# Kernel tuning notes

Hardware: AMD Instinct MI355X
Metric: run time of the kernel (lower is better)

Reference implementation:

```python
import jax, jax.numpy as jnp
import numpy as np

N_NODES = 100000
N_EDGES = 3200000
N_GRAPHS = 1000


def transformer_conv(x, src, dst, Wq, bq, Wk, bk, Wv, bv, Ws, bs, num_nodes):
    """PyG TransformerConv, heads=1, concat=True, root_weight=True, beta=False.
    Message flows src -> dst; softmax over incoming edges of each dst node."""
    d = Wq.shape[1]
    q = x @ Wq + bq                                   # [N, d]
    k = x @ Wk + bk                                   # [N, d]
    v = x @ Wv + bv                                   # [N, d]
    s = (q[dst] * k[src]).sum(-1) / jnp.sqrt(jnp.asarray(d, x.dtype))  # [E]
    smax = jax.ops.segment_max(s, dst, num_segments=num_nodes)         # [N]
    smax = jnp.where(jnp.isfinite(smax), smax, 0.0)   # nodes with no in-edges
    e = jnp.exp(s - smax[dst])                        # [E]
    denom = jax.ops.segment_sum(e, dst, num_segments=num_nodes)        # [N]
    alpha = e / jnp.maximum(denom[dst], 1e-16)        # [E]
    agg = jax.ops.segment_sum(alpha[:, None] * v[src], dst, num_segments=num_nodes)
    return agg + x @ Ws + bs                          # skip connection (lin_skip)


def setup_inputs() -> dict:
    key = jax.random.key(0)
    ks = jax.random.split(key, 20)
    x = jax.random.normal(ks[0], (N_NODES, 11), dtype=jnp.float32)
    edge_index = jax.random.randint(ks[1], (2, N_EDGES), 0, N_NODES, dtype=jnp.int64)
    batch = jnp.sort(jax.random.randint(ks[2], (N_NODES,), 0, N_GRAPHS, dtype=jnp.int64))

    def lin(k, fan_in, fan_out):
        kw, kb = jax.random.split(k)
        s = 1.0 / np.sqrt(fan_in)
        W = jax.random.uniform(kw, (fan_in, fan_out), jnp.float32, -s, s)
        b = jax.random.uniform(kb, (fan_out,), jnp.float32, -s, s)
        return W, b

    Wq1, bq1 = lin(ks[3], 11, 16); Wk1, bk1 = lin(ks[4], 11, 16)
    Wv1, bv1 = lin(ks[5], 11, 16); Ws1, bs1 = lin(ks[6], 11, 16)
    Wq2, bq2 = lin(ks[7], 16, 32); Wk2, bk2 = lin(ks[8], 16, 32)
    Wv2, bv2 = lin(ks[9], 16, 32); Ws2, bs2 = lin(ks[10], 16, 32)
    Wf1, bf1 = lin(ks[11], 32, 64)
    Wf2, bf2 = lin(ks[12], 64, 1)
    return dict(x=x, edge_index=edge_index, batch=batch,
                Wq1=Wq1, bq1=bq1, Wk1=Wk1, bk1=bk1, Wv1=Wv1, bv1=bv1, Ws1=Ws1, bs1=bs1,
                Wq2=Wq2, bq2=bq2, Wk2=Wk2, bk2=bk2, Wv2=Wv2, bv2=bv2, Ws2=Ws2, bs2=bs2,
                Wf1=Wf1, bf1=bf1, Wf2=Wf2, bf2=bf2)


def reference(x, edge_index, batch,
              Wq1, bq1, Wk1, bk1, Wv1, bv1, Ws1, bs1,
              Wq2, bq2, Wk2, bk2, Wv2, bv2, Ws2, bs2,
              Wf1, bf1, Wf2, bf2):
    src, dst = edge_index[0], edge_index[1]
    h = jax.nn.relu(transformer_conv(x, src, dst, Wq1, bq1, Wk1, bk1, Wv1, bv1, Ws1, bs1, N_NODES))
    h = jax.nn.relu(transformer_conv(h, src, dst, Wq2, bq2, Wk2, bk2, Wv2, bv2, Ws2, bs2, N_NODES))
    # global_mean_pool over graphs
    sums = jax.ops.segment_sum(h, batch, num_segments=N_GRAPHS)            # [G, 32]
    counts = jax.ops.segment_sum(jnp.ones((h.shape[0],), h.dtype), batch, num_segments=N_GRAPHS)
    g = sums / jnp.maximum(counts, 1.0)[:, None]
    g = jax.nn.relu(g @ Wf1 + bf1)
    return g @ Wf2 + bf2                                                   # [G, 1]
```

## Files before the change

kernel.cpp:

```cpp
#include <hip/hip_runtime.h>
#include <hip/hip_bf16.h>
#include <math.h>

#define N_NODES  100000
#define N_EDGES  3200000
#define N_GRAPHS 1000
#define NBKT ((N_NODES + 255) >> 8)
#define BCAP 9216
#define PCHUNK 4096
#define EPT (PCHUNK / 256)

__device__ __forceinline__ unsigned short f2bf(float f) {
    unsigned u = __float_as_uint(f);
    return (unsigned short)((u + 0x7FFFu + ((u >> 16) & 1u)) >> 16);
}
__device__ __forceinline__ void unpack2(unsigned u, float& a, float& b) {
    a = __uint_as_float(u << 16);
    b = __uint_as_float(u & 0xFFFF0000u);
}

__global__ void detect_kernel(const long long* __restrict__ idx, int* __restrict__ flag) {
    int t = threadIdx.x;
    unsigned long long hi = ((unsigned long long)idx[t]) >> 32;
    unsigned long long any = __ballot(hi != 0ull);
    if (t == 0) *flag = (any == 0ull) ? 1 : 0;
}

__global__ __launch_bounds__(256)
void init_kernel(unsigned* __restrict__ bcur, float* __restrict__ pool,
                 float* __restrict__ cnt) {
    int t = blockIdx.x * blockDim.x + threadIdx.x;
    if (t < NBKT)         bcur[t] = (unsigned)t * BCAP;
    if (t < N_GRAPHS*32)  pool[t] = 0.f;
    if (t < N_GRAPHS)     cnt[t]  = 0.f;
}

__global__ __launch_bounds__(256)
void partition_kernel(const int* __restrict__ idx32, const long long* __restrict__ idx64,
                      const int* __restrict__ flag,
                      unsigned* __restrict__ bcur, unsigned* __restrict__ srtp) {
    __shared__ unsigned       sbuf[PCHUNK];
    __shared__ unsigned short sbkt[PCHUNK];
    __shared__ unsigned lhist[NBKT];
    __shared__ unsigned lscan[512];
    __shared__ unsigned gbase[NBKT];
    const int is64 = *flag;
    const int t = threadIdx.x;
    const int base = blockIdx.x * PCHUNK;
    const int nval = min(PCHUNK, N_EDGES - base);

    for (int b = t; b < NBKT; b += 256) lhist[b] = 0u;
    __syncthreads();

    unsigned pr[EPT]; unsigned short br[EPT]; unsigned short rr[EPT];
    #pragma unroll
    for (int r = 0; r < EPT; ++r) {
        int e = base + r * 256 + t;
        br[r] = 0xFFFF;
        if (e < N_EDGES) {
            int s = is64 ? (int)idx64[e]           : idx32[e];
            int d = is64 ? (int)idx64[N_EDGES + e] : idx32[N_EDGES + e];
            unsigned bk = ((unsigned)d) >> 8;
            pr[r] = (((unsigned)d & 255u) << 17) | (unsigned)s;
            br[r] = (unsigned short)bk;
            rr[r] = (unsigned short)atomicAdd(&lhist[bk], 1u);
        }
    }
    __syncthreads();

    lscan[t]       = (t < NBKT)       ? lhist[t]       : 0u;
    lscan[t + 256] = (t + 256 < NBKT) ? lhist[t + 256] : 0u;
    __syncthreads();
    for (int off = 1; off < 512; off <<= 1) {
        unsigned v0 = (t >= off)       ? lscan[t - off]       : 0u;
        unsigned v1 = (t + 256 >= off) ? lscan[t + 256 - off] : 0u;
        __syncthreads();
        lscan[t] += v0; lscan[t + 256] += v1;
        __syncthreads();
    }

    for (int b = t; b < NBKT; b += 256) {
        unsigned c = lhist[b];
        if (c) gbase[b] = atomicAdd(&bcur[b], c);
    }

    #pragma unroll
    for (int r = 0; r < EPT; ++r) {
        if (br[r] != 0xFFFF) {
            unsigned b = br[r];
            unsigned slot = lscan[b] - lhist[b] + rr[r];
            sbuf[slot] = pr[r];
            sbkt[slot] = (unsigned short)b;
        }
    }
    __syncthreads();

    for (int slot = t; slot < nval; slot += 256) {
        unsigned p = sbuf[slot];
        unsigned b = sbkt[slot];
        unsigned lst = lscan[b] - lhist[b];
        srtp[gbase[b] + ((unsigned)slot - lst)] = p;
    }
}

__global__ __launch_bounds__(256)
void build_kernel(unsigned* __restrict__ srtp, const unsigned* __restrict__ bcur,
                  int* __restrict__ row_start, int* __restrict__ row_end) {
    __shared__ unsigned sbuf[BCAP];
    __shared__ int      sdst[BCAP];
    __shared__ unsigned ldeg[256];
    __shared__ unsigned lsc[256];
    __shared__ int      lcur[256];
    const int b = blockIdx.x;
    const int t = threadIdx.x;
    const int segbase = b * BCAP;
    const int cntb = min((int)bcur[b] - segbase, BCAP);

    ldeg[t] = 0u;
    __syncthreads();
    for (int e = t; e < cntb; e += 256) {
        unsigned p = srtp[segbase + e];
        sbuf[e] = p;
        atomicAdd(&ldeg[p >> 17], 1u);
    }
    __syncthreads();
    lsc[t] = ldeg[t];
    __syncthreads();
    for (int off = 1; off < 256; off <<= 1) {
        unsigned v = (t >= off) ? lsc[t - off] : 0u;
        __syncthreads();
        lsc[t] += v;
        __syncthreads();
    }
    int excl = (int)(lsc[t] - ldeg[t]);
    int node = (b << 8) + t;
    if (node < N_NODES) {
        row_start[node] = segbase + excl;
        row_end[node]   = segbase + excl + (int)ldeg[t];
    }
    lcur[t] = excl;
    __syncthreads();
    for (int e = t; e < cntb; e += 256) {
        unsigned p = sbuf[e];
        int pos = atomicAdd(&lcur[p >> 17], 1);
        sdst[pos] = (int)(p & 0x1FFFFu);
    }
    __syncthreads();

    const int wave = t >> 6, lane = t & 63;
    for (int n = wave; n < 256; n += 4) {
        int len = (int)ldeg[n];
        if (len < 2 || len > 64) continue;
        int lofs = (int)(lsc[n] - ldeg[n]);
        int v = (lane < len) ? sdst[lofs + lane] : 0x7FFFFFFF;
        #pragma unroll
        for (int k = 2; k <= 64; k <<= 1) {
            #pragma unroll
            for (int j = k >> 1; j > 0; j >>= 1) {
                int pv = __shfl_xor(v, j, 64);
                bool up    = (lane & k) == 0;
                bool lower = (lane & j) == 0;
                int mn = min(v, pv), mx = max(v, pv);
                v = (up == lower) ? mn : mx;
            }
        }
        if (lane < len) sdst[lofs + lane] = v;
    }
    __syncthreads();
    for (int e = t; e < cntb; e += 256)
        srtp[segbase + e] = (unsigned)sdst[e];
}

template <int IN, int OUT>
__global__ __launch_bounds__(256)
void lin_kernel(const float* __restrict__ x,
                const float* __restrict__ Wq, const float* __restrict__ bq,
                const float* __restrict__ Wk, const float* __restrict__ bk,
                const float* __restrict__ Wv, const float* __restrict__ bv,
                const float* __restrict__ Ws, const float* __restrict__ bs,
                float scale,
                float* __restrict__ q, unsigned short* __restrict__ kv,
                float* __restrict__ sk, int n)
{
    __shared__ float w[4 * IN * OUT];
    __shared__ float b[4 * OUT];
    for (int t = threadIdx.x; t < IN * OUT; t += blockDim.x) {
        w[t]            = Wq[t];
        w[IN*OUT + t]   = Wk[t];
        w[2*IN*OUT + t] = Wv[t];
        w[3*IN*OUT + t] = Ws[t];
    }
    for (int t = threadIdx.x; t < OUT; t += blockDim.x) {
        b[t]         = bq[t];
        b[OUT + t]   = bk[t];
        b[2*OUT + t] = bv[t];
        b[3*OUT + t] = bs[t];
    }
    __syncthreads();

    for (int i = blockIdx.x * blockDim.x + threadIdx.x; i < n;
         i += gridDim.x * blockDim.x) {
        float xi[IN];
        #pragma unroll
        for (int r = 0; r < IN; ++r) xi[r] = x[(size_t)i * IN + r];

        #pragma unroll
        for (int j = 0; j < OUT; ++j) {
            float aq = b[j], ak = b[OUT + j], av = b[2*OUT + j], as = b[3*OUT + j];
            #pragma unroll
            for (int r = 0; r < IN; ++r) {
                float xr = xi[r];
                aq += xr * w[r*OUT + j];
                ak += xr * w[IN*OUT + r*OUT + j];
                av += xr * w[2*IN*OUT + r*OUT + j];
                as += xr * w[3*IN*OUT + r*OUT + j];
            }
            int c = j >> 2, r4 = j & 3;
            q[(size_t)i * OUT + j]                  = aq * scale;
            kv[(size_t)i * 2 * OUT + c * 8 + r4]     = f2bf(ak);
            kv[(size_t)i * 2 * OUT + c * 8 + 4 + r4] = f2bf(av);
            sk[(size_t)i * OUT + j]                 = as;
        }
    }
}

template <int D, bool POOL>
__global__ __launch_bounds__(256)
void fused_attn_kernel(const float* __restrict__ q, const unsigned short* __restrict__ kv,
                       const float* __restrict__ sk,
                       const int* __restrict__ row_start, const int* __restrict__ row_end,
                       const unsigned* __restrict__ sorted_src,
                       const int* __restrict__ b32, const long long* __restrict__ b64,
                       const int* __restrict__ flag,
                       float* __restrict__ h, float* __restrict__ pool,
                       float* __restrict__ cnt)
{
    constexpr int L = D / 4;
    const int gpb = 256 / L;
    const int lj = threadIdx.x & (L - 1);
    int i = blockIdx.x * gpb + threadIdx.x / L;
    if (i >= N_NODES) return;

    const float4 qj = *(const float4*)(q + (size_t)i * D + lj * 4);
    const int beg = row_start[i], end = row_end[i];

    float m = -INFINITY, denom = 0.f;
    float4 acc = make_float4(0.f, 0.f, 0.f, 0.f);

    if (beg < end) {
        const int last = end - 1;

        int s0 = (int)sorted_src[min(beg + 0, last)];
        int s1 = (int)sorted_src[min(beg + 1, last)];
        int s2 = (int)sorted_src[min(beg + 2, last)];
        int s3 = (int)sorted_src[min(beg + 3, last)];
        uint4 A0 = ((const uint4*)(kv + (size_t)s0 * (2 * D)))[lj];
        uint4 A1 = ((const uint4*)(kv + (size_t)s1 * (2 * D)))[lj];
        uint4 B0 = ((const uint4*)(kv + (size_t)s2 * (2 * D)))[lj];
        uint4 B1 = ((const uint4*)(kv + (size_t)s3 * (2 * D)))[lj];

        for (int e = beg; e < end; e += 4) {
            {
                int sn0 = (int)sorted_src[min(e + 4, last)];
                int sn1 = (int)sorted_src[min(e + 5, last)];
                float k0,k1,k2,k3, l0,l1,l2,l3;
                unpack2(A0.x, k0, k1); unpack2(A0.y, k2, k3);
                unpack2(A1.x, l0, l1); unpack2(A1.y, l2, l3);
                float pa = k0*qj.x + k1*qj.y + k2*qj.z + k3*qj.w;
                float pb = l0*qj.x + l1*qj.y + l2*qj.z + l3*qj.w;
                #pragma unroll
                for (int off = L / 2; off; off >>= 1) {
                    pa += __shfl_xor(pa, off, L);
                    pb += __shfl_xor(pb, off, L);
                }
                if (e + 1 > last) pb = -INFINITY;
                float mn = fmaxf(m, fmaxf(pa, pb));
                float so = __expf(m - mn);
                float w0 = __expf(pa - mn);
                float w1 = __expf(pb - mn);
                float u0,u1,u2,u3, t0,t1,t2,t3;
                unpack2(A0.z, u0, u1); unpack2(A0.w, u2, u3);
                unpack2(A1.z, t0, t1); unpack2(A1.w, t2, t3);
                denom = denom * so + w0 + w1;
                acc.x = acc.x * so + w0 * u0 + w1 * t0;
                acc.y = acc.y * so + w0 * u1 + w1 * t1;
                acc.z = acc.z * so + w0 * u2 + w1 * t2;
                acc.w = acc.w * so + w0 * u3 + w1 * t3;
                m = mn;
                A0 = ((const uint4*)(kv + (size_t)sn0 * (2 * D)))[lj];
                A1 = ((const uint4*)(kv + (size_t)sn1 * (2 * D)))[lj];
            }
            {
                int sn0 = (int)sorted_src[min(e + 6, last)];
                int sn1 = (int)sorted_src[min(e + 7, last)];
                float k0,k1,k2,k3, l0,l1,l2,l3;
                unpack2(B0.x, k0, k1); unpack2(B0.y, k2, k3);
                unpack2(B1.x, l0, l1); unpack2(B1.y, l2, l3);
                float pa = k0*qj.x + k1*qj.y + k2*qj.z + k3*qj.w;
                float pb = l0*qj.x + l1*qj.y + l2*qj.z + l3*qj.w;
                #pragma unroll
                for (int off = L / 2; off; off >>= 1) {
                    pa += __shfl_xor(pa, off, L);
                    pb += __shfl_xor(pb, off, L);
                }
                if (e + 2 > last) pa = -INFINITY;
                if (e + 3 > last) pb = -INFINITY;
                float mn = fmaxf(m, fmaxf(pa, pb));
                float so = __expf(m - mn);
                float w0 = __expf(pa - mn);
                float w1 = __expf(pb - mn);
                float u0,u1,u2,u3, t0,t1,t2,t3;
                unpack2(B0.z, u0, u1); unpack2(B0.w, u2, u3);
                unpack2(B1.z, t0, t1); unpack2(B1.w, t2, t3);
                denom = denom * so + w0 + w1;
                acc.x = acc.x * so + w0 * u0 + w1 * t0;
                acc.y = acc.y * so + w0 * u1 + w1 * t1;
                acc.z = acc.z * so + w0 * u2 + w1 * t2;
                acc.w = acc.w * so + w0 * u3 + w1 * t3;
                m = mn;
                B0 = ((const uint4*)(kv + (size_t)sn0 * (2 * D)))[lj];
                B1 = ((const uint4*)(kv + (size_t)sn1 * (2 * D)))[lj];
            }
        }
    }

    float dn = 1.f / fmaxf(denom, 1e-16f);
    const float4 skv = *(const float4*)(sk + (size_t)i * D + lj * 4);
    float4 o;
    o.x = fmaxf(acc.x * dn + skv.x, 0.f);
    o.y = fmaxf(acc.y * dn + skv.y, 0.f);
    o.z = fmaxf(acc.z * dn + skv.z, 0.f);
    o.w = fmaxf(acc.w * dn + skv.w, 0.f);

    if (POOL) {
        int b = (*flag) ? (int)b64[i] : b32[i];
        float* pb = pool + b * 32 + lj * 4;
        atomicAdd(pb + 0, o.x);
        atomicAdd(pb + 1, o.y);
        atomicAdd(pb + 2, o.z);
        atomicAdd(pb + 3, o.w);
        if (lj == 0) atomicAdd(&cnt[b], 1.f);
    } else {
        *(float4*)(h + (size_t)i * D + lj * 4) = o;
    }
}

__global__ __launch_bounds__(64)
void mlp_kernel(const float* __restrict__ pool, const float* __restrict__ cnt,
                const float* __restrict__ Wf1, const float* __restrict__ bf1,
                const float* __restrict__ Wf2, const float* __restrict__ bf2,
                float* __restrict__ out)
{
    int g = blockIdx.x;
    int h = threadIdx.x;
    __shared__ float m[32];
    if (h < 32) {
        float c = fmaxf(cnt[g], 1.f);
        m[h] = pool[g * 32 + h] / c;
    }
    __syncthreads();
    float acc = bf1[h];
    #pragma unroll
    for (int r = 0; r < 32; ++r) acc += m[r] * Wf1[r * 64 + h];
    float hid = fmaxf(acc, 0.f);
    float c = hid * Wf2[h];
    #pragma unroll
    for (int off = 32; off; off >>= 1) c += __shfl_xor(c, off, 64);
    if (h == 0) out[g] = c + bf2[0];
}

extern "C" void kernel_launch(void* const* d_in, const int* in_sizes, int n_in,
                              void* d_out, int out_size, void* d_ws, size_t ws_size,
                              hipStream_t stream) {
    const float* x = (const float*)d_in[0];
    const void*  edge_index = d_in[1];
    const void*  batch      = d_in[2];
    const float* Wq1 = (const float*)d_in[3];  const float* bq1 = (const float*)d_in[4];
    const float* Wk1 = (const float*)d_in[5];  const float* bk1 = (const float*)d_in[6];
    const float* Wv1 = (const float*)d_in[7];  const float* bv1 = (const float*)d_in[8];
    const float* Ws1 = (const float*)d_in[9];  const float* bs1 = (const float*)d_in[10];
    const float* Wq2 = (const float*)d_in[11]; const float* bq2 = (const float*)d_in[12];
    const float* Wk2 = (const float*)d_in[13]; const float* bk2 = (const float*)d_in[14];
    const float* Wv2 = (const float*)d_in[15]; const float* bv2 = (const float*)d_in[16];
    const float* Ws2 = (const float*)d_in[17]; const float* bs2 = (const float*)d_in[18];
    const float* Wf1 = (const float*)d_in[19]; const float* bf1 = (const float*)d_in[20];
    const float* Wf2 = (const float*)d_in[21]; const float* bf2 = (const float*)d_in[22];
    float* out = (float*)d_out;

    char* ws = (char*)d_ws;
    size_t off = 0;
    auto carve = [&](size_t bytes) {
        char* p = ws + off;
        off = (off + bytes + 255) & ~(size_t)255;
        return p;
    };
    int*            flag     = (int*)            carve(16);
    int*            row_start= (int*)            carve((size_t)N_NODES * 4);
    int*            row_end  = (int*)            carve((size_t)N_NODES * 4);
    unsigned*       bcur     = (unsigned*)       carve((size_t)NBKT * 4);
    float*          pool     = (float*)          carve((size_t)N_GRAPHS * 32 * 4);
    float*          cnt      = (float*)          carve((size_t)N_GRAPHS * 4);
    unsigned*       srtp     = (unsigned*)       carve((size_t)NBKT * BCAP * 4);
    float*          qb       = (float*)          carve((size_t)N_NODES * 32 * 4);
    unsigned short* kvb      = (unsigned short*) carve((size_t)N_NODES * 64 * 2);
    float*          skb      = (float*)          carve((size_t)N_NODES * 32 * 4);
    float*          h1       = (float*)          carve((size_t)N_NODES * 16 * 4);
    (void)ws_size; (void)in_sizes; (void)n_in; (void)out_size;

    const int* ei32 = (const int*)edge_index;
    const long long* ei64 = (const long long*)edge_index;
    const int* b32 = (const int*)batch;
    const long long* b64 = (const long long*)batch;

    const dim3 blk(256);

    detect_kernel<<<1, 64, 0, stream>>>(ei64, flag);
    init_kernel<<<(N_GRAPHS * 32 + 255) / 256, blk, 0, stream>>>(bcur, pool, cnt);
    partition_kernel<<<(N_EDGES + PCHUNK - 1) / PCHUNK, blk, 0, stream>>>(
        ei32, ei64, flag, bcur, srtp);
    build_kernel<<<NBKT, blk, 0, stream>>>(srtp, bcur, row_start, row_end);

    lin_kernel<11, 16><<<(N_NODES + 255) / 256, blk, 0, stream>>>(
        x, Wq1, bq1, Wk1, bk1, Wv1, bv1, Ws1, bs1, 0.25f,
        qb, kvb, skb, N_NODES);
    fused_attn_kernel<16, false><<<(N_NODES + 63) / 64, blk, 0, stream>>>(
        qb, kvb, skb, row_start, row_end, srtp, b32, b64, flag, h1, pool, cnt);

    lin_kernel<16, 32><<<(N_NODES + 255) / 256, blk, 0, stream>>>(
        h1, Wq2, bq2, Wk2, bk2, Wv2, bv2, Ws2, bs2, 0.17677669529663688f,
        qb, kvb, skb, N_NODES);
    fused_attn_kernel<32, true><<<(N_NODES + 31) / 32, blk, 0, stream>>>(
        qb, kvb, skb, row_start, row_end, srtp, b32, b64, flag, nullptr, pool, cnt);

    mlp_kernel<<<N_GRAPHS, 64, 0, stream>>>(pool, cnt, Wf1, bf1, Wf2, bf2, out);
}
```

Measured before the change: 397.7 us.

## Reorder attention nodes by in-degree to balance work within wavefronts

Adds a degree histogram in the CSR build, a single-thread scan, and a scatter kernel that builds a permutation grouping nodes by in-degree (highest first). Both attention kernels then process nodes through this permutation, so each wavefront handles nodes with similar edge counts. The aim is less divergence and better load balance from uneven degrees. The cost is two extra kernel launches, an extra indirection per node, and scattered writes and pool atomics, since neighbouring threads no longer work on consecutive nodes.

```diff
diff --git a/kernel.cpp b/kernel.cpp
--- a/kernel.cpp
+++ b/kernel.cpp
@@ -9,6 +9,7 @@
 #define BCAP 9216
 #define PCHUNK 4096
 #define EPT (PCHUNK / 256)
+#define DBIN 128
 
 __device__ __forceinline__ unsigned short f2bf(float f) {
     unsigned u = __float_as_uint(f);
@@ -28,11 +29,12 @@
 
 __global__ __launch_bounds__(256)
 void init_kernel(unsigned* __restrict__ bcur, float* __restrict__ pool,
-                 float* __restrict__ cnt) {
+                 float* __restrict__ cnt, unsigned* __restrict__ dh) {
     int t = blockIdx.x * blockDim.x + threadIdx.x;
     if (t < NBKT)         bcur[t] = (unsigned)t * BCAP;
     if (t < N_GRAPHS*32)  pool[t] = 0.f;
     if (t < N_GRAPHS)     cnt[t]  = 0.f;
+    if (t < DBIN)         dh[t]   = 0u;
 }
 
 __global__ __launch_bounds__(256)
@@ -105,7 +107,8 @@
 
 __global__ __launch_bounds__(256)
 void build_kernel(unsigned* __restrict__ srtp, const unsigned* __restrict__ bcur,
-                  int* __restrict__ row_start, int* __restrict__ row_end) {
+                  int* __restrict__ row_start, int* __restrict__ row_end,
+                  unsigned* __restrict__ dh) {
     __shared__ unsigned sbuf[BCAP];
     __shared__ int      sdst[BCAP];
     __shared__ unsigned ldeg[256];
@@ -137,6 +140,7 @@
     if (node < N_NODES) {
         row_start[node] = segbase + excl;
         row_end[node]   = segbase + excl + (int)ldeg[t];
+        atomicAdd(&dh[min((int)ldeg[t], DBIN - 1)], 1u);
     }
     lcur[t] = excl;
     __syncthreads();
@@ -171,6 +175,23 @@
         srtp[segbase + e] = (unsigned)sdst[e];
 }
 
+__global__ void degscan_kernel(const unsigned* __restrict__ dh, unsigned* __restrict__ dcur) {
+    if (threadIdx.x == 0) {
+        unsigned acc = 0;
+        for (int d = DBIN - 1; d >= 0; --d) { dcur[d] = acc; acc += dh[d]; }
+    }
+}
+
+__global__ __launch_bounds__(256)
+void degscatter_kernel(const int* __restrict__ row_start, const int* __restrict__ row_end,
+                       unsigned* __restrict__ dcur, int* __restrict__ perm) {
+    int i = blockIdx.x * blockDim.x + threadIdx.x;
+    if (i >= N_NODES) return;
+    int d = min(row_end[i] - row_start[i], DBIN - 1);
+    unsigned pos = atomicAdd(&dcur[d], 1u);
+    perm[pos] = i;
+}
+
 template <int IN, int OUT>
 __global__ __launch_bounds__(256)
 void lin_kernel(const float* __restrict__ x,
@@ -230,6 +251,7 @@
                        const float* __restrict__ sk,
                        const int* __restrict__ row_start, const int* __restrict__ row_end,
                        const unsigned* __restrict__ sorted_src,
+                       const int* __restrict__ perm,
                        const int* __restrict__ b32, const long long* __restrict__ b64,
                        const int* __restrict__ flag,
                        float* __restrict__ h, float* __restrict__ pool,
@@ -238,8 +260,9 @@
     constexpr int L = D / 4;
     const int gpb = 256 / L;
     const int lj = threadIdx.x & (L - 1);
-    int i = blockIdx.x * gpb + threadIdx.x / L;
-    if (i >= N_NODES) return;
+    int g = blockIdx.x * gpb + threadIdx.x / L;
+    if (g >= N_NODES) return;
+    const int i = perm[g];
 
     const float4 qj = *(const float4*)(q + (size_t)i * D + lj * 4);
     const int beg = row_start[i], end = row_end[i];
@@ -400,6 +423,9 @@
     unsigned*       bcur     = (unsigned*)       carve((size_t)NBKT * 4);
     float*          pool     = (float*)          carve((size_t)N_GRAPHS * 32 * 4);
     float*          cnt      = (float*)          carve((size_t)N_GRAPHS * 4);
+    unsigned*       dh       = (unsigned*)       carve((size_t)DBIN * 4);
+    unsigned*       dcur     = (unsigned*)       carve((size_t)DBIN * 4);
+    int*            perm     = (int*)            carve((size_t)N_NODES * 4);
     unsigned*       srtp     = (unsigned*)       carve((size_t)NBKT * BCAP * 4);
     float*          qb       = (float*)          carve((size_t)N_NODES * 32 * 4);
     unsigned short* kvb      = (unsigned short*) carve((size_t)N_NODES * 64 * 2);
@@ -415,22 +441,25 @@
     const dim3 blk(256);
 
     detect_kernel<<<1, 64, 0, stream>>>(ei64, flag);
-    init_kernel<<<(N_GRAPHS * 32 + 255) / 256, blk, 0, stream>>>(bcur, pool, cnt);
+    init_kernel<<<(N_GRAPHS * 32 + 255) / 256, blk, 0, stream>>>(bcur, pool, cnt, dh);
     partition_kernel<<<(N_EDGES + PCHUNK - 1) / PCHUNK, blk, 0, stream>>>(
         ei32, ei64, flag, bcur, srtp);
-    build_kernel<<<NBKT, blk, 0, stream>>>(srtp, bcur, row_start, row_end);
+    build_kernel<<<NBKT, blk, 0, stream>>>(srtp, bcur, row_start, row_end, dh);
+    degscan_kernel<<<1, 64, 0, stream>>>(dh, dcur);
+    degscatter_kernel<<<(N_NODES + 255) / 256, blk, 0, stream>>>(
+        row_start, row_end, dcur, perm);
 
     lin_kernel<11, 16><<<(N_NODES + 255) / 256, blk, 0, stream>>>(
         x, Wq1, bq1, Wk1, bk1, Wv1, bv1, Ws1, bs1, 0.25f,
         qb, kvb, skb, N_NODES);
     fused_attn_kernel<16, false><<<(N_NODES + 63) / 64, blk, 0, stream>>>(
-        qb, kvb, skb, row_start, row_end, srtp, b32, b64, flag, h1, pool, cnt);
+        qb, kvb, skb, row_start, row_end, srtp, perm, b32, b64, flag, h1, pool, cnt);
 
     lin_kernel<16, 32><<<(N_NODES + 255) / 256, blk, 0, stream>>>(
         h1, Wq2, bq2, Wk2, bk2, Wv2, bv2, Ws2, bs2, 0.17677669529663688f,
         qb, kvb, skb, N_NODES);
     fused_attn_kernel<32, true><<<(N_NODES + 31) / 32, blk, 0, stream>>>(
-        qb, kvb, skb, row_start, row_end, srtp, b32, b64, flag, nullptr, pool, cnt);
+        qb, kvb, skb, row_start, row_end, srtp, perm, b32, b64, flag, nullptr, pool, cnt);
 
     mlp_kernel<<<N_GRAPHS, 64, 0, stream>>>(pool, cnt, Wf1, bf1, Wf2, bf2, out);
 }
```

After: 678.9 us. 1.71x slower.
